# Kernel optimization log

Hardware: AMD Instinct MI355X
Metric: run time of the kernel (lower is better)

Reference implementation:

```python
import jax, jax.numpy as jnp
import numpy as np

NUM_CLASSES = 80
S = 7            # grid_size
NB = 2           # num_boxes per cell
LAMBDA_COORD = 5.0
LAMBDA_NOOBJ = 0.5
N_BOX = 20       # padded boxes per image


def setup_inputs() -> dict:
    key = jax.random.key(0)
    k1, k2, k3, k4 = jax.random.split(key, 4)
    B = 4096
    predictions = jax.random.uniform(k1, (B, S, S, NB, 5 + NUM_CLASSES), dtype=jnp.float32)
    # build valid normalized xyxy boxes: centers in [0.1,0.9], half-sizes in [0.01,0.085]
    centers = jax.random.uniform(k2, (B, N_BOX, 2), dtype=jnp.float32) * 0.8 + 0.1
    half = jax.random.uniform(k3, (B, N_BOX, 2), dtype=jnp.float32) * 0.075 + 0.01
    targets_boxes = jnp.concatenate([centers - half, centers + half], axis=-1)
    targets_labels = jax.random.randint(k4, (B, N_BOX), 0, NUM_CLASSES)
    return {"predictions": predictions, "targets_boxes": targets_boxes, "targets_labels": targets_labels}


def encode_targets(boxes, labels):
    # boxes: [B,N,4] xyxy normalized; labels: [B,N] int
    B, N, _ = boxes.shape
    x = (boxes[..., 0] + boxes[..., 2]) * 0.5
    y = (boxes[..., 1] + boxes[..., 3]) * 0.5
    w = boxes[..., 2] - boxes[..., 0]
    h = boxes[..., 3] - boxes[..., 1]
    j = jnp.clip(jnp.floor(x * S).astype(jnp.int32), 0, S - 1)
    i = jnp.clip(jnp.floor(y * S).astype(jnp.int32), 0, S - 1)
    x_cell = x * S - j
    y_cell = y * S - i
    onehot = jax.nn.one_hot(labels, NUM_CLASSES, dtype=boxes.dtype)
    feats = jnp.concatenate([x_cell[..., None], y_cell[..., None], w[..., None], h[..., None],
                             jnp.ones_like(x_cell)[..., None], onehot], axis=-1)  # [B,N,5+C]
    bidx = jnp.arange(B, dtype=jnp.int32)[:, None]
    flat = ((bidx * S + i) * S + j).ravel()                       # [B*N] cell ids
    order = jnp.broadcast_to(jnp.arange(N, dtype=jnp.int32), (B, N)).ravel()
    winner = jnp.full((B * S * S,), N, dtype=jnp.int32).at[flat].min(order)
    cell_b = jnp.arange(B * S * S, dtype=jnp.int32) // (S * S)
    sel = jnp.minimum(winner, N - 1)
    grid = feats[cell_b, sel]
    grid = jnp.where((winner < N)[:, None], grid, jnp.zeros_like(grid))
    return grid.reshape(B, S, S, 5 + NUM_CLASSES)


def iou_xywh(a, b):
    ax1 = a[..., 0] - a[..., 2] * 0.5; ay1 = a[..., 1] - a[..., 3] * 0.5
    ax2 = a[..., 0] + a[..., 2] * 0.5; ay2 = a[..., 1] + a[..., 3] * 0.5
    bx1 = b[..., 0] - b[..., 2] * 0.5; by1 = b[..., 1] - b[..., 3] * 0.5
    bx2 = b[..., 0] + b[..., 2] * 0.5; by2 = b[..., 1] + b[..., 3] * 0.5
    iw = jnp.clip(jnp.minimum(ax2, bx2) - jnp.maximum(ax1, bx1), 0.0)
    ih = jnp.clip(jnp.minimum(ay2, by2) - jnp.maximum(ay1, by1), 0.0)
    inter = iw * ih
    union = (ax2 - ax1) * (ay2 - ay1) + (bx2 - bx1) * (by2 - by1) - inter
    return inter / (union + 1e-6)


def yolo_loss(predictions, targets_boxes, targets_labels):
    B = predictions.shape[0]
    tg = encode_targets(targets_boxes, targets_labels)   # [B,S,S,5+C]
    txy, twh = tg[..., :2], tg[..., 2:4]
    tconf, tcls = tg[..., 4:5], tg[..., 5:]
    obj = (tconf[..., 0] > 0).astype(predictions.dtype)   # [B,S,S]
    # responsible box = argmax IoU per cell, masked by obj
    pred_boxes = predictions[..., 0:4]                     # [B,S,S,NB,4]
    tgt_boxes = jnp.concatenate([txy, twh], axis=-1)[:, :, :, None, :]
    ious = iou_xywh(pred_boxes, jnp.broadcast_to(tgt_boxes, pred_boxes.shape))  # [B,S,S,NB]
    best = jnp.argmax(ious, axis=-1)
    resp = jax.nn.one_hot(best, NB, dtype=predictions.dtype) * obj[..., None]   # [B,S,S,NB]
    pxy = predictions[..., 0:2]; pwh = predictions[..., 2:4]
    pconf = predictions[..., 4:5]; pcls = predictions[..., 5:]
    om = obj[..., None, None]        # [B,S,S,1,1]
    rm = resp[..., None]             # [B,S,S,NB,1]
    loss_xy = LAMBDA_COORD * jnp.sum(om * rm * (pxy - txy[:, :, :, None, :]) ** 2) / B
    loss_wh = LAMBDA_COORD * jnp.sum(om * rm * (jnp.sqrt(jnp.clip(pwh, 1e-6)) - jnp.sqrt(jnp.clip(twh[:, :, :, None, :], 1e-6))) ** 2) / B
    loss_conf_obj = jnp.sum(om * rm * (pconf - tconf[:, :, :, None, :]) ** 2) / B
    loss_conf_noobj = LAMBDA_NOOBJ * jnp.sum((1.0 - obj)[..., None, None] * pconf ** 2) / B
    pred_cls_resp = jnp.sum(pcls * rm, axis=3)             # [B,S,S,C]
    loss_cls = jnp.sum(obj[..., None] * (pred_cls_resp - tcls) ** 2) / B
    return loss_xy + loss_wh + loss_conf_obj + loss_conf_noobj + loss_cls


def reference(predictions, targets_boxes, targets_labels):
    return yolo_loss(predictions, targets_boxes, targets_labels)
```

## Files before the change

### kernel.cpp

```cpp
#include <hip/hip_runtime.h>

#define S 7
#define NB 2
#define NC 80
#define NBOX 20
#define CELLS 49
#define CH 85
#define PAIR 170
#define PER_B 8330
#define NIMG 4096
#define NCELL_TOT (NIMG*CELLS)
#define N4TOT (NIMG*PER_B/4)
#define PREP_IMGS 4
#define PREP_BLOCKS (NIMG/PREP_IMGS)
#define STREAM_BLOCKS 2048
#define TSTRIDE (STREAM_BLOCKS*256)
#define L_COORD 5.0f
#define L_NOOBJ 0.5f

__device__ __forceinline__ void block_reduce_store(float acc, float* dst)
{
    __shared__ float s_wsum[4];
    int tid = threadIdx.x;
    #pragma unroll
    for (int off = 32; off > 0; off >>= 1) acc += __shfl_down(acc, off, 64);
    int lane = tid & 63, wv = tid >> 6;
    if (lane == 0) s_wsum[wv] = acc;
    __syncthreads();
    if (tid == 0) *dst = s_wsum[0] + s_wsum[1] + s_wsum[2] + s_wsum[3];
}

__global__ __launch_bounds__(256) void prep_kernel(
    const float* __restrict__ pred,
    const float* __restrict__ boxes,
    const int*   __restrict__ labels,
    float4*      __restrict__ wt4,
    float*       __restrict__ partial)
{
    __shared__ int   s_winner[PREP_IMGS * CELLS];
    __shared__ float s_cx[PREP_IMGS * NBOX], s_cy[PREP_IMGS * NBOX];
    __shared__ float s_bw[PREP_IMGS * NBOX], s_bh[PREP_IMGS * NBOX];
    __shared__ int   s_lab[PREP_IMGS * NBOX];

    const int b0  = blockIdx.x * PREP_IMGS;
    const int tid = threadIdx.x;

    if (tid < PREP_IMGS * CELLS) s_winner[tid] = NBOX;
    __syncthreads();

    if (tid < PREP_IMGS * NBOX) {
        int img = tid / NBOX, bxi = tid - img * NBOX;
        const float* bx = boxes + ((size_t)(b0 + img) * NBOX + bxi) * 4;
        float x1 = bx[0], y1 = bx[1], x2 = bx[2], y2 = bx[3];
        float x = (x1 + x2) * 0.5f, y = (y1 + y2) * 0.5f;
        s_cx[tid] = x; s_cy[tid] = y;
        s_bw[tid] = x2 - x1; s_bh[tid] = y2 - y1;
        s_lab[tid] = labels[(size_t)(b0 + img) * NBOX + bxi];
        int j = (int)floorf(x * (float)S); j = min(max(j, 0), S - 1);
        int i = (int)floorf(y * (float)S); i = min(max(i, 0), S - 1);
        atomicMin(&s_winner[img * CELLS + i * S + j], bxi);
    }
    __syncthreads();

    float acc = 0.0f;
    if (tid < PREP_IMGS * CELLS) {
        int img  = tid / CELLS;
        int cell = tid - img * CELLS;
        int w    = s_winner[tid];
        float4 wq;
        if (w < NBOX) {
            int i = cell / S, j = cell - (cell / S) * S;
            int bi = img * NBOX + w;
            float x = s_cx[bi], y = s_cy[bi];
            float tx = x * (float)S - (float)j;
            float ty = y * (float)S - (float)i;
            float tw = s_bw[bi], th = s_bh[bi];

            const float* p = pred + ((size_t)(b0 + img) * CELLS + cell) * PAIR;
            float bx1 = tx - tw * 0.5f, by1 = ty - th * 0.5f;
            float bx2 = tx + tw * 0.5f, by2 = ty + th * 0.5f;
            float barea = (bx2 - bx1) * (by2 - by1);
            float iou[2], px[2], py[2], pw[2], ph[2];
            #pragma unroll
            for (int nb = 0; nb < NB; nb++) {
                px[nb] = p[nb * CH + 0]; py[nb] = p[nb * CH + 1];
                pw[nb] = p[nb * CH + 2]; ph[nb] = p[nb * CH + 3];
                float ax1 = px[nb] - pw[nb] * 0.5f, ay1 = py[nb] - ph[nb] * 0.5f;
                float ax2 = px[nb] + pw[nb] * 0.5f, ay2 = py[nb] + ph[nb] * 0.5f;
                float iw = fmaxf(fminf(ax2, bx2) - fmaxf(ax1, bx1), 0.0f);
                float ih = fmaxf(fminf(ay2, by2) - fmaxf(ay1, by1), 0.0f);
                float inter = iw * ih;
                float uni = (ax2 - ax1) * (ay2 - ay1) + barea - inter;
                iou[nb] = inter / (uni + 1e-6f);
            }
            int resp = (iou[1] > iou[0]) ? 1 : 0;
            wq = (resp == 0) ? make_float4(1.f, 1.f, 0.f, 0.f)
                             : make_float4(0.f, 0.f, 1.f, 1.f);

            float pc = p[resp * CH + 4];
            float pl = p[resp * CH + 5 + s_lab[bi]];
            float dx = px[resp] - tx, dy = py[resp] - ty;
            float dw = sqrtf(fmaxf(pw[resp], 1e-6f)) - sqrtf(fmaxf(tw, 1e-6f));
            float dh = sqrtf(fmaxf(ph[resp], 1e-6f)) - sqrtf(fmaxf(th, 1e-6f));
            acc = L_COORD * (dx * dx + dy * dy + dw * dw + dh * dh)
                + (1.0f - 2.0f * pc)
                + (1.0f - 2.0f * pl);
        } else {
            wq = make_float4(L_NOOBJ, 0.f, L_NOOBJ, 0.f);
        }
        wt4[(size_t)(b0 + img) * CELLS + cell] = wq;
    }
    __syncthreads();
    block_reduce_store(acc, &partial[blockIdx.x]);
}

__device__ __forceinline__ float elem1(float p, int r, float4 w)
{
    int nb = (r >= CH) ? 1 : 0;
    int rr = r - nb * CH;
    float wconf = nb ? w.z : w.x;
    float wcls  = nb ? w.w : w.y;
    float m = (rr >= 5) ? wcls : ((rr == 4) ? wconf : 0.0f);
    return m * p * p;
}

__device__ __forceinline__ float elem4(float4 v, int e,
                                       const float4* __restrict__ wt4)
{
    unsigned ff = 4u * (unsigned)e;
    unsigned c0 = ff / (unsigned)PAIR;
    int r0 = (int)(ff - c0 * (unsigned)PAIR);
    float4 w0 = wt4[c0];
    float4 w1 = w0;
    bool wrap = (r0 == PAIR - 2);
    if (wrap) w1 = wt4[c0 + 1];
    int r2 = wrap ? 0 : r0 + 2;
    float a;
    a  = elem1(v.x, r0,     w0);
    a += elem1(v.y, r0 + 1, w0);
    a += elem1(v.z, r2,     w1);
    a += elem1(v.w, r2 + 1, w1);
    return a;
}

__global__ __launch_bounds__(256) void stream_kernel(
    const float4* __restrict__ p4,
    const float4* __restrict__ wt4,
    float*        __restrict__ partial)
{
    const int tid = threadIdx.x;
    const int gid = blockIdx.x * 256 + tid;

    float acc = 0.0f;
    int e = gid;
    #pragma unroll 8
    for (int k = 0; k < 16; ++k) {
        acc += elem4(p4[e], e, wt4);
        e += TSTRIDE;
    }
    if (e < N4TOT) acc += elem4(p4[e], e, wt4);

    block_reduce_store(acc, &partial[blockIdx.x]);
}

__global__ __launch_bounds__(256) void reduce_kernel(
    const float* __restrict__ partial, int n,
    float* __restrict__ out, float inv_B)
{
    const int tid = threadIdx.x;
    float acc = 0.0f;
    for (int i = tid; i < n; i += 256) acc += partial[i];
    __shared__ float s_wsum[4];
    #pragma unroll
    for (int off = 32; off > 0; off >>= 1) acc += __shfl_down(acc, off, 64);
    int lane = tid & 63, wv = tid >> 6;
    if (lane == 0) s_wsum[wv] = acc;
    __syncthreads();
    if (tid == 0) out[0] = (s_wsum[0] + s_wsum[1] + s_wsum[2] + s_wsum[3]) * inv_B;
}

extern "C" void kernel_launch(void* const* d_in, const int* in_sizes, int n_in,
                              void* d_out, int out_size, void* d_ws, size_t ws_size,
                              hipStream_t stream) {
    const float* pred   = (const float*)d_in[0];
    const float* boxes  = (const float*)d_in[1];
    const int*   labels = (const int*)d_in[2];

    float4* wt4          = (float4*)d_ws;
    float*  prep_part    = (float*)d_ws + (size_t)NCELL_TOT * 4;
    float*  stream_part  = prep_part + PREP_BLOCKS;

    prep_kernel<<<PREP_BLOCKS, 256, 0, stream>>>(pred, boxes, labels, wt4, prep_part);
    stream_kernel<<<STREAM_BLOCKS, 256, 0, stream>>>((const float4*)pred, wt4, stream_part);
    reduce_kernel<<<1, 256, 0, stream>>>(prep_part, PREP_BLOCKS + STREAM_BLOCKS,
                                         (float*)d_out, 1.0f / (float)NIMG);
}
```

Baseline: 201.9 us.

## Simplify stream weights to per-box scalars and move noobj/coord corrections into prep

The stream kernel now squares every prediction element and weights it by a single per-box scalar, so it needs only one or two scalar weight loads and a compare per float4. The previous per-element channel masking and float4 weight table go away. To keep the result exact, the prep kernel subtracts the xywh squares of the responsible box and adds the noobj confidence term directly. Each block now reads a contiguous chunk with nontemporal loads instead of a grid-strided pattern, and the grid shape changes to 1960 blocks of 17 iterations. In exchange, the stream kernel does extra multiply-adds on channels that were previously masked out, and the final sum relies on cancellation of those extra terms.

Result: no change. 204.6 us (+1.4%).

```diff
diff --git a/kernel.cpp b/kernel.cpp
--- a/kernel.cpp
+++ b/kernel.cpp
@@ -9,14 +9,16 @@
 #define PAIR 170
 #define PER_B 8330
 #define NIMG 4096
-#define NCELL_TOT (NIMG*CELLS)
+#define NBOXSLOT (NIMG*CELLS*NB)
 #define N4TOT (NIMG*PER_B/4)
 #define PREP_IMGS 4
 #define PREP_BLOCKS (NIMG/PREP_IMGS)
-#define STREAM_BLOCKS 2048
-#define TSTRIDE (STREAM_BLOCKS*256)
+#define STREAM_BLOCKS 1960
+#define STREAM_ITERS 17
 #define L_COORD 5.0f
 #define L_NOOBJ 0.5f
+
+typedef float vfloat4 __attribute__((ext_vector_type(4)));
 
 __device__ __forceinline__ void block_reduce_store(float acc, float* dst)
 {
@@ -34,7 +36,7 @@
     const float* __restrict__ pred,
     const float* __restrict__ boxes,
     const int*   __restrict__ labels,
-    float4*      __restrict__ wt4,
+    float*       __restrict__ wb,
     float*       __restrict__ partial)
 {
     __shared__ int   s_winner[PREP_IMGS * CELLS];
@@ -67,7 +69,9 @@
         int img  = tid / CELLS;
         int cell = tid - img * CELLS;
         int w    = s_winner[tid];
-        float4 wq;
+        size_t slot = ((size_t)(b0 + img) * CELLS + cell) * 2;
+        const float* p = pred + ((size_t)(b0 + img) * CELLS + cell) * PAIR;
+        float w0 = 0.f, w1 = 0.f;
         if (w < NBOX) {
             int i = cell / S, j = cell - (cell / S) * S;
             int bi = img * NBOX + w;
@@ -76,7 +80,6 @@
             float ty = y * (float)S - (float)i;
             float tw = s_bw[bi], th = s_bh[bi];
 
-            const float* p = pred + ((size_t)(b0 + img) * CELLS + cell) * PAIR;
             float bx1 = tx - tw * 0.5f, by1 = ty - th * 0.5f;
             float bx2 = tx + tw * 0.5f, by2 = ty + th * 0.5f;
             float barea = (bx2 - bx1) * (by2 - by1);
@@ -94,8 +97,8 @@
                 iou[nb] = inter / (uni + 1e-6f);
             }
             int resp = (iou[1] > iou[0]) ? 1 : 0;
-            wq = (resp == 0) ? make_float4(1.f, 1.f, 0.f, 0.f)
-                             : make_float4(0.f, 0.f, 1.f, 1.f);
+            w0 = (resp == 0) ? 1.f : 0.f;
+            w1 = 1.f - w0;
 
             float pc = p[resp * CH + 4];
             float pl = p[resp * CH + 5 + s_lab[bi]];
@@ -104,62 +107,47 @@
             float dh = sqrtf(fmaxf(ph[resp], 1e-6f)) - sqrtf(fmaxf(th, 1e-6f));
             acc = L_COORD * (dx * dx + dy * dy + dw * dw + dh * dh)
                 + (1.0f - 2.0f * pc)
-                + (1.0f - 2.0f * pl);
+                + (1.0f - 2.0f * pl)
+                - (px[resp] * px[resp] + py[resp] * py[resp]
+                 + pw[resp] * pw[resp] + ph[resp] * ph[resp]);
         } else {
-            wq = make_float4(L_NOOBJ, 0.f, L_NOOBJ, 0.f);
+            float c0 = p[4], c1 = p[CH + 4];
+            acc = L_NOOBJ * (c0 * c0 + c1 * c1);
         }
-        wt4[(size_t)(b0 + img) * CELLS + cell] = wq;
+        wb[slot]     = w0;
+        wb[slot + 1] = w1;
     }
     __syncthreads();
     block_reduce_store(acc, &partial[blockIdx.x]);
 }
 
-__device__ __forceinline__ float elem1(float p, int r, float4 w)
+__global__ __launch_bounds__(256) void stream_kernel(
+    const vfloat4* __restrict__ p4,
+    const float*   __restrict__ wb,
+    float*         __restrict__ partial)
 {
-    int nb = (r >= CH) ? 1 : 0;
-    int rr = r - nb * CH;
-    float wconf = nb ? w.z : w.x;
-    float wcls  = nb ? w.w : w.y;
-    float m = (rr >= 5) ? wcls : ((rr == 4) ? wconf : 0.0f);
-    return m * p * p;
-}
-
-__device__ __forceinline__ float elem4(float4 v, int e,
-                                       const float4* __restrict__ wt4)
-{
-    unsigned ff = 4u * (unsigned)e;
-    unsigned c0 = ff / (unsigned)PAIR;
-    int r0 = (int)(ff - c0 * (unsigned)PAIR);
-    float4 w0 = wt4[c0];
-    float4 w1 = w0;
-    bool wrap = (r0 == PAIR - 2);
-    if (wrap) w1 = wt4[c0 + 1];
-    int r2 = wrap ? 0 : r0 + 2;
-    float a;
-    a  = elem1(v.x, r0,     w0);
-    a += elem1(v.y, r0 + 1, w0);
-    a += elem1(v.z, r2,     w1);
-    a += elem1(v.w, r2 + 1, w1);
-    return a;
-}
-
-__global__ __launch_bounds__(256) void stream_kernel(
-    const float4* __restrict__ p4,
-    const float4* __restrict__ wt4,
-    float*        __restrict__ partial)
-{
-    const int tid = threadIdx.x;
-    const int gid = blockIdx.x * 256 + tid;
+    const int tid  = threadIdx.x;
+    const int base = blockIdx.x * (STREAM_ITERS * 256);
 
     float acc = 0.0f;
-    int e = gid;
-    #pragma unroll 8
-    for (int k = 0; k < 16; ++k) {
-        acc += elem4(p4[e], e, wt4);
-        e += TSTRIDE;
+    #pragma unroll
+    for (int k = 0; k < STREAM_ITERS; ++k) {
+        int e = base + k * 256 + tid;
+        vfloat4 v = __builtin_nontemporal_load(&p4[e]);
+        unsigned ff = 4u * (unsigned)e;
+        unsigned bi = ff / 85u;
+        int r85 = (int)(ff - bi * 85u);
+        int thr = 85 - r85;
+        float wa = wb[bi];
+        float wn = wb[bi + 1];
+        float w1 = (1 < thr) ? wa : wn;
+        float w2 = (2 < thr) ? wa : wn;
+        float w3 = (3 < thr) ? wa : wn;
+        acc += wa * (v.x * v.x);
+        acc += w1 * (v.y * v.y);
+        acc += w2 * (v.z * v.z);
+        acc += w3 * (v.w * v.w);
     }
-    if (e < N4TOT) acc += elem4(p4[e], e, wt4);
-
     block_reduce_store(acc, &partial[blockIdx.x]);
 }
 
@@ -186,12 +174,12 @@
     const float* boxes  = (const float*)d_in[1];
     const int*   labels = (const int*)d_in[2];
 
-    float4* wt4          = (float4*)d_ws;
-    float*  prep_part    = (float*)d_ws + (size_t)NCELL_TOT * 4;
-    float*  stream_part  = prep_part + PREP_BLOCKS;
+    float* wb          = (float*)d_ws;
+    float* prep_part   = wb + NBOXSLOT + 16;
+    float* stream_part = prep_part + PREP_BLOCKS;
 
-    prep_kernel<<<PREP_BLOCKS, 256, 0, stream>>>(pred, boxes, labels, wt4, prep_part);
-    stream_kernel<<<STREAM_BLOCKS, 256, 0, stream>>>((const float4*)pred, wt4, stream_part);
+    prep_kernel<<<PREP_BLOCKS, 256, 0, stream>>>(pred, boxes, labels, wb, prep_part);
+    stream_kernel<<<STREAM_BLOCKS, 256, 0, stream>>>((const vfloat4*)pred, wb, stream_part);
     reduce_kernel<<<1, 256, 0, stream>>>(prep_part, PREP_BLOCKS + STREAM_BLOCKS,
                                          (float*)d_out, 1.0f / (float)NIMG);
 }
```
